# Optimization experiments

Hardware: AMD Instinct MI355X
Metric: run time of the kernel (lower is better)

Reference implementation:

```python
import jax, jax.numpy as jnp
import numpy as np

ALPHA = 1.0
BETA = 0.5
B, N, T = 4096, 32, 8
EPS = 1e-8


def _lsa_square(cost):
    """Jonker-Volgenant shortest augmenting path LSA on a square cost [n,n].
    Returns col_of_row[i] = column assigned to row i (same as scipy's
    linear_sum_assignment col_ind for square matrices)."""
    n = cost.shape[0]
    INF = np.inf
    u = np.zeros(n + 1)
    v = np.zeros(n + 1)
    p = np.zeros(n + 1, dtype=np.int64)   # p[j] = row matched to column j (1-based)
    way = np.zeros(n + 1, dtype=np.int64)
    for i in range(1, n + 1):
        p[0] = i
        j0 = 0
        minv = np.full(n + 1, INF)
        used = np.zeros(n + 1, dtype=bool)
        while True:
            used[j0] = True
            i0 = p[j0]
            # vectorized relaxation over all unused columns
            cur = cost[i0 - 1] - u[i0] - v[1:]
            free = ~used[1:]
            mv = minv[1:]
            wy = way[1:]
            upd = free & (cur < mv)
            mv[upd] = cur[upd]
            wy[upd] = j0
            masked = np.where(free, mv, INF)
            j1 = int(np.argmin(masked)) + 1
            delta = masked[j1 - 1]
            u[p[used]] += delta
            v[used] -= delta
            minv[~used] -= delta
            j0 = j1
            if p[j0] == 0:
                break
        while j0:
            j1 = way[j0]
            p[j0] = p[j1]
            j0 = j1
    col_of_row = np.empty(n, dtype=np.int32)
    for j in range(1, n + 1):
        col_of_row[p[j] - 1] = j - 1
    return col_of_row


def _batched_lsa(cost):
    cost = np.asarray(cost, dtype=np.float64)
    return np.stack([_lsa_square(c) for c in cost]).astype(np.int32)


def hungarian(cost):
    b, n = cost.shape[0], cost.shape[1]
    return jax.pure_callback(_batched_lsa, jax.ShapeDtypeStruct((b, n), jnp.int32), cost)


def _assignment(pred_j, logits, target_j, target_types):
    # j_cost[b,i,j] = |pred_j[b,i] - target_j[b,j]|
    j_cost = jnp.abs(pred_j[:, :, None] - target_j[:, None, :])
    # torch code uses -log(softmax + 1e-8) for the cost matrix (not log_softmax)
    logp = jnp.log(jax.nn.softmax(logits, axis=-1) + EPS)      # [B,N,T]
    idx = jnp.broadcast_to(target_types[:, None, :].astype(jnp.int32), j_cost.shape)
    type_cost = -jnp.take_along_axis(logp, idx, axis=-1)       # [B,N,N]
    cost = ALPHA * j_cost + BETA * type_cost
    return hungarian(jax.lax.stop_gradient(cost))              # [B,N] int32


def _matched_loss(pred_j, logits, target_j, target_types, cols):
    # row_ind == arange(N) for square full-mask case; cols = assigned targets
    tj = jnp.take_along_axis(target_j, cols.astype(jnp.int32), axis=1)        # [B,N]
    tt = jnp.take_along_axis(target_types, cols.astype(jnp.int64), axis=1)    # [B,N]
    j_loss = jnp.abs(pred_j - tj).sum()
    ls = jax.nn.log_softmax(logits, axis=-1)
    type_loss = -jnp.take_along_axis(ls, tt[..., None].astype(jnp.int32), axis=-1).sum()
    total = pred_j.shape[0] * pred_j.shape[1]
    loss = (ALPHA * j_loss + BETA * type_loss) / total
    j_mae = j_loss / total
    type_acc = (jnp.argmax(logits, axis=-1) == tt).astype(jnp.float32).mean()
    return loss, j_mae, type_acc


def setup_inputs() -> dict:
    key = jax.random.key(0)
    k1, k2, k3, k4 = jax.random.split(key, 4)
    return {
        'pred_j': jax.random.normal(k1, (B, N), dtype=jnp.float32),
        'pred_type_logits': jax.random.normal(k2, (B, N, T), dtype=jnp.float32),
        'target_j': jax.random.normal(k3, (B, N), dtype=jnp.float32),
        'target_types': jax.random.randint(k4, (B, N), 0, T, dtype=jnp.int64),
        'pred_mask': jnp.ones((B, N), dtype=bool),
        'target_mask': jnp.ones((B, N), dtype=bool),
    }


def reference(pred_j, pred_type_logits, target_j, target_types, pred_mask, target_mask):
    # Masks are all-ones here, so every slot is valid and the per-sample
    # torch loop vectorizes into one batched computation (same math).
    cols = _assignment(pred_j, pred_type_logits, target_j, target_types)
    loss, j_mae, type_acc = _matched_loss(pred_j, pred_type_logits, target_j, target_types, cols)
    return loss, j_mae, type_acc
```

## Files before the change

kernel.cpp:

```cpp
#include <hip/hip_runtime.h>
#include <math.h>


constexpr int BB = 4096;
constexpr int NN = 32;
constexpr int TT = 8;
constexpr float ALPHA_F = 1.0f;
constexpr float BETA_F  = 0.5f;
constexpr float EPS_F   = 1e-8f;

typedef float f32x32 __attribute__((ext_vector_type(32)));

template <int CTRL, int ROW_MASK>
__device__ __forceinline__ float dpp_min(float x) {
    int t = __builtin_amdgcn_update_dpp(__float_as_int(x), __float_as_int(x),
                                        CTRL, ROW_MASK, 0xf, false);
    return fminf(x, __int_as_float(t));
}

__device__ __forceinline__ float wave32_min_bcast(float x) {
    x = dpp_min<0xB1,  0xf>(x);
    x = dpp_min<0x4E,  0xf>(x);
    x = dpp_min<0x124, 0xf>(x);
    x = dpp_min<0x128, 0xf>(x);
    x = dpp_min<0x142, 0xa>(x);
    return __int_as_float(__builtin_amdgcn_readlane(__float_as_int(x), 31));
}

__device__ __forceinline__ float readlane_f(float x, int lane) {
    return __int_as_float(__builtin_amdgcn_readlane(__float_as_int(x), lane));
}

__global__ __launch_bounds__(256) void hungarian_lsa_kernel(
    const float* __restrict__ pred_j,
    const float* __restrict__ logits,
    const float* __restrict__ target_j,
    const int*   __restrict__ target_types,
    double* __restrict__ partials)
{
    __shared__ float lgpS[4][NN * TT];
    __shared__ float lgtS[4][NN * TT];

    const int wave = threadIdx.x >> 6;
    const int lane = threadIdx.x & 63;
    const int col  = lane & 31;
    const int b    = blockIdx.x * 4 + wave;

    float* lgp = lgpS[wave];
    float* lgt = lgtS[wave];

    const float pj = pred_j  [b * NN + col];
    const float tj = target_j[b * NN + col];
    const int   tt = target_types[b * NN + col];

    float x[TT];
    const float* lrow = logits + ((size_t)b * NN + col) * TT;
#pragma unroll
    for (int t = 0; t < TT; ++t) x[t] = lrow[t];

    float m = x[0]; int am = 0;
#pragma unroll
    for (int t = 1; t < TT; ++t) { if (x[t] > m) { m = x[t]; am = t; } }
    float s = 0.f;
#pragma unroll
    for (int t = 0; t < TT; ++t) s += expf(x[t] - m);
    const float lse = m + logf(s);

    if (lane < 32) {
#pragma unroll
        for (int t = 0; t < TT; ++t) {
            float p = expf(x[t] - m) / s;
            lgp[col * TT + t] = logf(p + EPS_F);
            lgt[col * TT + t] = x[t];
        }
    }
    __syncthreads();

    int p_m1 = 0;
    if (lane < 32) {
        f32x32 cc;
#pragma unroll
        for (int r = 0; r < NN; ++r) {
            const float pjr = readlane_f(pj, r);
            const float lp  = lgp[r * TT + tt];
            cc[r] = ALPHA_F * fabsf(pjr - tj) + BETA_F * (-lp);
        }

        const float INFF = __builtin_inff();
        float negv = 0.f;
        float ucf  = 0.f;
        unsigned amask = 0u;

        for (int i = 1; i <= NN; ++i) {
            float vmask = 0.f;
            float snap  = 0.f;
            float curm  = cc[i - 1] + negv;
            float mv    = wave32_min_bcast(curm);
            unsigned long long bm = __ballot(curm == mv);
            int   j1m1  = __ffsll(bm) - 1;
            float rowSum = mv;

            while ((amask >> j1m1) & 1u) {
                const bool isJ = (col == j1m1);
                snap  = isJ ? rowSum : snap;
                vmask = isJ ? INFF   : vmask;
                const float u_curV = readlane_f(ucf, j1m1);
                const int   r0     = __builtin_amdgcn_readlane(p_m1, j1m1);
                curm = (cc[r0] + negv) + vmask;
                mv   = wave32_min_bcast(curm);
                bm   = __ballot(curm == mv);
                j1m1 = __ffsll(bm) - 1;
                rowSum += mv - u_curV;
            }

            const bool isJ = (col == j1m1);
            p_m1 = isJ ? (i - 1) : p_m1;
            const float dv  = rowSum - snap;
            const float dvj = (vmask > 0.f) ? dv : 0.f;
            negv += dvj;
            ucf  += dvj;
            ucf   = isJ ? rowSum : ucf;
            amask |= 1u << j1m1;
        }
    }

    const int   row      = p_m1;
    const float pj_row   = __shfl(pj,  row);
    const float lse_row  = __shfl(lse, row);
    const int   am_row   = __shfl(am,  row);
    const float logit_tt = lgt[row * TT + tt];

    double sj = (lane < 32) ? (double)fabsf(pj_row - tj)   : 0.0;
    double st = (lane < 32) ? (double)(lse_row - logit_tt) : 0.0;
    double sa = (lane < 32) ? ((am_row == tt) ? 1.0 : 0.0) : 0.0;
#pragma unroll
    for (int off = 32; off >= 1; off >>= 1) {
        sj += __shfl_xor(sj, off);
        st += __shfl_xor(st, off);
        sa += __shfl_xor(sa, off);
    }
    if (lane == 0) {
        partials[b * 3 + 0] = sj;
        partials[b * 3 + 1] = st;
        partials[b * 3 + 2] = sa;
    }
}

__global__ __launch_bounds__(256) void hungarian_finalize_kernel(
    const double* __restrict__ partials, float* __restrict__ out)
{
    __shared__ double sm0[256], sm1[256], sm2[256];
    const int tid = threadIdx.x;
    double a = 0.0, c = 0.0, e = 0.0;
    for (int i = tid; i < BB; i += 256) {
        a += partials[i * 3 + 0];
        c += partials[i * 3 + 1];
        e += partials[i * 3 + 2];
    }
    sm0[tid] = a; sm1[tid] = c; sm2[tid] = e;
    __syncthreads();
    for (int s = 128; s > 0; s >>= 1) {
        if (tid < s) {
            sm0[tid] += sm0[tid + s];
            sm1[tid] += sm1[tid + s];
            sm2[tid] += sm2[tid + s];
        }
        __syncthreads();
    }
    if (tid == 0) {
        const double jl = sm0[0], tl = sm1[0], ac = sm2[0];
        const double total = (double)BB * (double)NN;
        out[0] = (float)((jl + 0.5 * tl) / total);
        out[1] = (float)(jl / total);
        out[2] = (float)(ac / total);
    }
}

extern "C" void kernel_launch(void* const* d_in, const int* in_sizes, int n_in,
                              void* d_out, int out_size, void* d_ws, size_t ws_size,
                              hipStream_t stream) {
    const float* pred_j       = (const float*)d_in[0];
    const float* logits       = (const float*)d_in[1];
    const float* target_j     = (const float*)d_in[2];
    const int*   target_types = (const int*)  d_in[3];

    double* partials = (double*)d_ws;
    float*  out      = (float*)d_out;

    hungarian_lsa_kernel<<<BB / 4, 256, 0, stream>>>(
        pred_j, logits, target_j, target_types, partials);
    hungarian_finalize_kernel<<<1, 256, 0, stream>>>(partials, out);
}
```

Before: 47.56 us.

## Fuse finalize into LSA kernel via last-block atomic and tighten inner loop masking

The separate finalize kernel is removed. Each block now increments a global counter after writing its partials, and the last block to arrive performs the reduction, which saves one kernel launch. A hipMemsetAsync is added to reset the counter on every call. The augmenting-path inner loop also replaces its select-based masking with inline v_cndmask on an SGPR lane mask and folds the INF mask into the negv copy, shortening the critical serial loop at the cost of relying on inline asm.

```diff
diff --git a/kernel.cpp b/kernel.cpp
--- a/kernel.cpp
+++ b/kernel.cpp
@@ -31,15 +31,24 @@
     return __int_as_float(__builtin_amdgcn_readlane(__float_as_int(x), lane));
 }
 
+__device__ __forceinline__ void cndmask_inplace(float& d, float t,
+                                                unsigned long long cm) {
+    asm("v_cndmask_b32 %0, %0, %1, %2" : "+v"(d) : "v"(t), "s"(cm));
+}
+
 __global__ __launch_bounds__(256) void hungarian_lsa_kernel(
     const float* __restrict__ pred_j,
     const float* __restrict__ logits,
     const float* __restrict__ target_j,
     const int*   __restrict__ target_types,
-    double* __restrict__ partials)
+    double* __restrict__ partials,
+    unsigned*   __restrict__ counter,
+    float*      __restrict__ out)
 {
     __shared__ float lgpS[4][NN * TT];
     __shared__ float lgtS[4][NN * TT];
+    __shared__ double sm0[256], sm1[256], sm2[256];
+    __shared__ int    lastFlag;
 
     const int wave = threadIdx.x >> 6;
     const int lane = threadIdx.x & 63;
@@ -87,36 +96,39 @@
         }
 
         const float INFF = __builtin_inff();
+        float vINF;
+        asm("v_mov_b32 %0, 0x7f800000" : "=v"(vINF));
         float negv = 0.f;
         float ucf  = 0.f;
         unsigned amask = 0u;
 
         for (int i = 1; i <= NN; ++i) {
-            float vmask = 0.f;
+            float nvm   = negv;
             float snap  = 0.f;
-            float curm  = cc[i - 1] + negv;
+            float curm  = cc[i - 1] + nvm;
             float mv    = wave32_min_bcast(curm);
             unsigned long long bm = __ballot(curm == mv);
             int   j1m1  = __ffsll(bm) - 1;
             float rowSum = mv;
 
             while ((amask >> j1m1) & 1u) {
-                const bool isJ = (col == j1m1);
-                snap  = isJ ? rowSum : snap;
-                vmask = isJ ? INFF   : vmask;
+                const unsigned long long cm = 1ull << j1m1;
+                cndmask_inplace(snap, rowSum, cm);
+                cndmask_inplace(nvm,  vINF,   cm);
                 const float u_curV = readlane_f(ucf, j1m1);
                 const int   r0     = __builtin_amdgcn_readlane(p_m1, j1m1);
-                curm = (cc[r0] + negv) + vmask;
+                curm = cc[r0] + nvm;
                 mv   = wave32_min_bcast(curm);
                 bm   = __ballot(curm == mv);
                 j1m1 = __ffsll(bm) - 1;
-                rowSum += mv - u_curV;
+                rowSum += mv;
+                rowSum -= u_curV;
             }
 
             const bool isJ = (col == j1m1);
             p_m1 = isJ ? (i - 1) : p_m1;
             const float dv  = rowSum - snap;
-            const float dvj = (vmask > 0.f) ? dv : 0.f;
+            const float dvj = (nvm == INFF) ? dv : 0.f;
             negv += dvj;
             ucf  += dvj;
             ucf   = isJ ? rowSum : ucf;
@@ -144,35 +156,39 @@
         partials[b * 3 + 1] = st;
         partials[b * 3 + 2] = sa;
     }
-}
-
-__global__ __launch_bounds__(256) void hungarian_finalize_kernel(
-    const double* __restrict__ partials, float* __restrict__ out)
-{
-    __shared__ double sm0[256], sm1[256], sm2[256];
-    const int tid = threadIdx.x;
-    double a = 0.0, c = 0.0, e = 0.0;
-    for (int i = tid; i < BB; i += 256) {
-        a += partials[i * 3 + 0];
-        c += partials[i * 3 + 1];
-        e += partials[i * 3 + 2];
-    }
-    sm0[tid] = a; sm1[tid] = c; sm2[tid] = e;
+
+    __threadfence();
+    if (threadIdx.x == 0) {
+        const unsigned old = atomicAdd(counter, 1u);
+        lastFlag = (old == (unsigned)(BB / 4 - 1));
+    }
     __syncthreads();
-    for (int s = 128; s > 0; s >>= 1) {
-        if (tid < s) {
-            sm0[tid] += sm0[tid + s];
-            sm1[tid] += sm1[tid + s];
-            sm2[tid] += sm2[tid + s];
-        }
+    if (lastFlag) {
+        __threadfence();
+        const int tid = threadIdx.x;
+        double a = 0.0, c = 0.0, e = 0.0;
+        for (int i = tid; i < BB; i += 256) {
+            a += partials[i * 3 + 0];
+            c += partials[i * 3 + 1];
+            e += partials[i * 3 + 2];
+        }
+        sm0[tid] = a; sm1[tid] = c; sm2[tid] = e;
         __syncthreads();
-    }
-    if (tid == 0) {
-        const double jl = sm0[0], tl = sm1[0], ac = sm2[0];
-        const double total = (double)BB * (double)NN;
-        out[0] = (float)((jl + 0.5 * tl) / total);
-        out[1] = (float)(jl / total);
-        out[2] = (float)(ac / total);
+        for (int sdx = 128; sdx > 0; sdx >>= 1) {
+            if (tid < sdx) {
+                sm0[tid] += sm0[tid + sdx];
+                sm1[tid] += sm1[tid + sdx];
+                sm2[tid] += sm2[tid + sdx];
+            }
+            __syncthreads();
+        }
+        if (tid == 0) {
+            const double jl = sm0[0], tl = sm1[0], ac = sm2[0];
+            const double total = (double)BB * (double)NN;
+            out[0] = (float)((jl + 0.5 * tl) / total);
+            out[1] = (float)(jl / total);
+            out[2] = (float)(ac / total);
+        }
     }
 }
 
@@ -184,10 +200,11 @@
     const float* target_j     = (const float*)d_in[2];
     const int*   target_types = (const int*)  d_in[3];
 
-    double* partials = (double*)d_ws;
-    float*  out      = (float*)d_out;
-
+    double*   partials = (double*)d_ws;
+    unsigned* counter  = (unsigned*)((char*)d_ws + BB * 3 * sizeof(double));
+    float*    out      = (float*)d_out;
+
+    hipMemsetAsync(counter, 0, sizeof(unsigned), stream);
     hungarian_lsa_kernel<<<BB / 4, 256, 0, stream>>>(
-        pred_j, logits, target_j, target_types, partials);
-    hungarian_finalize_kernel<<<1, 256, 0, stream>>>(partials, out);
-}
+        pred_j, logits, target_j, target_types, partials, counter, out);
+}
```

Measured after the change: 95.59 us. +101.0%, slower.
